# Performance work log

Hardware: AMD Instinct MI355X
Metric: run time of the kernel (lower is better)

The kernel has to match this reference:

```python
import jax, jax.numpy as jnp
import numpy as np

B, T, D, H, DH = 2, 2048, 1024, 16, 64
LN_EPS = 1e-5


def setup_inputs() -> dict:
    key = jax.random.key(0)
    ks = jax.random.split(key, 16)
    s = 0.02
    return {
        "query_sequences": jax.random.normal(ks[0], (B, T, D), jnp.float32),
        "key_sequences": jax.random.normal(ks[1], (B, T, D), jnp.float32),
        "value_sequences": jax.random.normal(ks[2], (B, T, D), jnp.float32),
        "key_value_sequence_lengths": jax.random.randint(ks[3], (B,), 1, T + 1),
        "Wq": jax.random.normal(ks[4], (D, H * DH), jnp.float32) * s,
        "bq": jnp.zeros((H * DH,), jnp.float32),
        "Wk": jax.random.normal(ks[5], (D, H * DH), jnp.float32) * s,
        "bk": jnp.zeros((H * DH,), jnp.float32),
        "Wv": jax.random.normal(ks[6], (D, H * DH), jnp.float32) * s,
        "bv": jnp.zeros((H * DH,), jnp.float32),
        "Wo": jax.random.normal(ks[7], (H * DH, D), jnp.float32) * s,
        "bo": jnp.zeros((D,), jnp.float32),
        "gamma": jnp.ones((D,), jnp.float32),
        "beta": jnp.zeros((D,), jnp.float32),
    }


def _layer_norm(x, gamma, beta):
    mu = jnp.mean(x, axis=-1, keepdims=True)
    var = jnp.var(x, axis=-1, keepdims=True)
    return (x - mu) * jax.lax.rsqrt(var + LN_EPS) * gamma + beta


def reference(query_sequences, key_sequences, value_sequences,
              key_value_sequence_lengths, Wq, bq, Wk, bk, Wv, bv, Wo, bo,
              gamma, beta):
    # pre-LN (self-attn: same LN applied to q, k, v inputs)
    q_in = _layer_norm(query_sequences, gamma, beta)
    k_in = _layer_norm(key_sequences, gamma, beta)
    v_in = _layer_norm(value_sequences, gamma, beta)

    # projections -> [B, H, T, DH]
    q = (q_in @ Wq + bq).reshape(B, T, H, DH).transpose(0, 2, 1, 3)
    k = (k_in @ Wk + bk).reshape(B, T, H, DH).transpose(0, 2, 1, 3)
    v = (v_in @ Wv + bv).reshape(B, T, H, DH).transpose(0, 2, 1, 3)

    scale = 1.0 / jnp.sqrt(jnp.float32(DH))
    scores = jnp.einsum('bhtd,bhTd->bhtT', q, k) * scale  # [B,H,Tq,Tk]

    # key padding mask: key position < sequence length
    pad_mask = jnp.arange(T)[None, None, None, :] < key_value_sequence_lengths[:, None, None, None]
    # causal mask (self_attn and in_decoder)
    causal = jnp.tril(jnp.ones((T, T), bool))[None, None]
    mask = pad_mask & causal
    scores = jnp.where(mask, scores, -jnp.inf)

    attn = jax.nn.softmax(scores, axis=-1)  # dropout=0 (eval)
    attn_viz = attn.reshape(B * H, T, T)

    out = jnp.einsum('bhtT,bhTd->bhtd', attn, v)
    out = out.transpose(0, 2, 1, 3).reshape(B, T, H * DH)
    out = out @ Wo + bo
    return out, attn_viz
```

## Files before the change

### kernel.cpp

```cpp
#include <hip/hip_runtime.h>
#include <hip/hip_bf16.h>

#define B_  2
#define T_  2048
#define D_  1024
#define H_  16
#define DH_ 64
#define M_  (B_*T_)

typedef __bf16 bf16;
typedef __bf16 bf16x8 __attribute__((ext_vector_type(8)));
typedef __bf16 bf16x4 __attribute__((ext_vector_type(4)));
typedef float  f32x4  __attribute__((ext_vector_type(4)));

#define SCL2 0.18033688011112042f

#define GLD16(g, l) __builtin_amdgcn_global_load_lds( \
    (const __attribute__((address_space(1))) void*)(g), \
    (__attribute__((address_space(3))) void*)(l), 16, 0, 0)

__global__ __launch_bounds__(256) void ln_kernel(
    const float* __restrict__ xq, const float* __restrict__ xk,
    const float* __restrict__ xv, const float* __restrict__ gamma,
    const float* __restrict__ beta,
    bf16* __restrict__ oq, bf16* __restrict__ ok, bf16* __restrict__ ov)
{
    const int row = blockIdx.x;
    const int sel = blockIdx.y;
    const float* x = (sel == 0 ? xq : sel == 1 ? xk : xv) + (size_t)row * D_;
    bf16*        o = (sel == 0 ? oq : sel == 1 ? ok : ov) + (size_t)row * D_;
    const int tid = threadIdx.x;

    float4 v = *(const float4*)&x[tid * 4];
    float s  = v.x + v.y + v.z + v.w;
    float s2 = v.x*v.x + v.y*v.y + v.z*v.z + v.w*v.w;
    for (int off = 32; off > 0; off >>= 1) {
        s  += __shfl_down(s,  off, 64);
        s2 += __shfl_down(s2, off, 64);
    }
    __shared__ float red[8];
    const int wave = tid >> 6, lane = tid & 63;
    if (lane == 0) { red[wave] = s; red[4 + wave] = s2; }
    __syncthreads();
    s  = red[0] + red[1] + red[2] + red[3];
    s2 = red[4] + red[5] + red[6] + red[7];
    const float mu   = s * (1.0f / D_);
    const float var  = s2 * (1.0f / D_) - mu * mu;
    const float rstd = rsqrtf(var + 1e-5f);

    float4 g  = *(const float4*)&gamma[tid * 4];
    float4 bb = *(const float4*)&beta[tid * 4];
    bf16x4 o4;
    o4[0] = (bf16)((v.x - mu) * rstd * g.x + bb.x);
    o4[1] = (bf16)((v.y - mu) * rstd * g.y + bb.y);
    o4[2] = (bf16)((v.z - mu) * rstd * g.z + bb.z);
    o4[3] = (bf16)((v.w - mu) * rstd * g.w + bb.w);
    *(bf16x4*)&o[tid * 4] = o4;
}

__global__ __launch_bounds__(256) void wconv_kernel(
    const float* __restrict__ Wq, const float* __restrict__ Wk,
    const float* __restrict__ Wv, const float* __restrict__ Wo,
    bf16* __restrict__ wqt, bf16* __restrict__ wkt,
    bf16* __restrict__ wvt, bf16* __restrict__ wot)
{
    const float* Ws[4] = {Wq, Wk, Wv, Wo};
    bf16*        Wt[4] = {wqt, wkt, wvt, wot};
    const float* W = Ws[blockIdx.z];
    bf16*        O = Wt[blockIdx.z];
    const int n0 = blockIdx.x * 32, k0 = blockIdx.y * 32;
    __shared__ float tile[32][33];
    const int tid = threadIdx.x;
    #pragma unroll
    for (int i = 0; i < 4; i++) {
        int e = tid + i * 256;
        int r = e >> 5, c = e & 31;
        tile[r][c] = W[(size_t)(k0 + r) * 1024 + n0 + c];
    }
    __syncthreads();
    #pragma unroll
    for (int i = 0; i < 4; i++) {
        int e = tid + i * 256;
        int nr = e >> 5, kc = e & 31;
        O[(size_t)(n0 + nr) * 1024 + k0 + kc] = (bf16)tile[kc][nr];
    }
}

__global__ __launch_bounds__(256) void vtrans_kernel(
    const bf16* __restrict__ Vh, bf16* __restrict__ VhT)
{
    const int bh = blockIdx.y, t0 = blockIdx.x * 64;
    const bf16* src = Vh  + (size_t)bh * T_ * DH_;
    bf16*       dst = VhT + (size_t)bh * T_ * DH_;
    __shared__ bf16 tile[64][72];
    const int tid = threadIdx.x;
    const int r = tid >> 3, c8 = (tid & 7) * 8;
    *(bf16x8*)&tile[r][c8]      = *(const bf16x8*)&src[(size_t)(t0 + r) * DH_ + c8];
    *(bf16x8*)&tile[32 + r][c8] = *(const bf16x8*)&src[(size_t)(t0 + 32 + r) * DH_ + c8];
    __syncthreads();
    bf16x8 o0, o1;
    #pragma unroll
    for (int j = 0; j < 8; j++) { o0[j] = tile[c8 + j][r]; o1[j] = tile[c8 + j][32 + r]; }
    *(bf16x8*)&dst[(size_t)r * T_ + t0 + c8]        = o0;
    *(bf16x8*)&dst[(size_t)(32 + r) * T_ + t0 + c8] = o1;
}

template <int MODE>
__global__ __launch_bounds__(256) void gemm_bt(
    const bf16* __restrict__ A, const bf16* __restrict__ Bt,
    const float* __restrict__ bias, void* __restrict__ Cout)
{
    __shared__ bf16 sA[128][32];
    __shared__ bf16 sB[128][32];
    const int tid  = threadIdx.x;
    const int wave = tid >> 6, lane = tid & 63;
    const int quad = lane >> 4, l16 = lane & 15;
    const int wr = (wave >> 1) * 64, wc = (wave & 1) * 64;
    const int m0 = blockIdx.y * 128, n0 = blockIdx.x * 128;

    f32x4 acc[4][4] = {};

    const int srow = wave * 32 + (lane >> 2);
    const int scol = (lane & 3) * 8;
    const bf16* gA0 = &A [(size_t)(m0 + srow)      * 1024 + scol];
    const bf16* gA1 = &A [(size_t)(m0 + srow + 16) * 1024 + scol];
    const bf16* gB0 = &Bt[(size_t)(n0 + srow)      * 1024 + scol];
    const bf16* gB1 = &Bt[(size_t)(n0 + srow + 16) * 1024 + scol];
    bf16* lA0 = &sA[wave * 32][0];
    bf16* lA1 = &sA[wave * 32 + 16][0];
    bf16* lB0 = &sB[wave * 32][0];
    bf16* lB1 = &sB[wave * 32 + 16][0];

    for (int k0 = 0; k0 < 1024; k0 += 32) {
        __syncthreads();
        GLD16(gA0 + k0, lA0);
        GLD16(gA1 + k0, lA1);
        GLD16(gB0 + k0, lB0);
        GLD16(gB1 + k0, lB1);
        __syncthreads();

        bf16x8 af[4], bfr[4];
        #pragma unroll
        for (int i = 0; i < 4; i++) af[i]  = *(bf16x8*)&sA[wr + i * 16 + l16][quad * 8];
        #pragma unroll
        for (int j = 0; j < 4; j++) bfr[j] = *(bf16x8*)&sB[wc + j * 16 + l16][quad * 8];
        #pragma unroll
        for (int i = 0; i < 4; i++)
            #pragma unroll
            for (int j = 0; j < 4; j++)
                acc[i][j] = __builtin_amdgcn_mfma_f32_16x16x32_bf16(af[i], bfr[j], acc[i][j], 0, 0, 0);
    }

    #pragma unroll
    for (int i = 0; i < 4; i++) {
        #pragma unroll
        for (int j = 0; j < 4; j++) {
            const int n = n0 + wc + j * 16 + l16;
            const float bia = bias[n];
            #pragma unroll
            for (int r = 0; r < 4; r++) {
                const int m = m0 + wr + i * 16 + quad * 4 + r;
                const float v = acc[i][j][r] + bia;
                if (MODE == 0) {
                    const int b = m >> 11, t = m & 2047, h = n >> 6, dh = n & 63;
                    ((bf16*)Cout)[(((size_t)b * H_ + h) * T_ + t) * DH_ + dh] = (bf16)v;
                } else {
                    ((float*)Cout)[(size_t)m * 1024 + n] = v;
                }
            }
        }
    }
}

__global__ __launch_bounds__(256) void attn_kernel(
    const bf16* __restrict__ Qh, const bf16* __restrict__ Kh,
    const bf16* __restrict__ VhT, const int* __restrict__ lens,
    float* __restrict__ attn_out, bf16* __restrict__ Obuf)
{
    const int bh = blockIdx.y;
    const int b = bh >> 4, h = bh & 15;
    const int bx = blockIdx.x;
    const int q0 = bx * 64;
    const int len = lens[b];
    const bf16* Qp = Qh  + (size_t)bh * T_ * DH_;
    const bf16* Kp = Kh  + (size_t)bh * T_ * DH_;
    const bf16* Vp = VhT + (size_t)bh * T_ * DH_;
    float* attnp = attn_out + (size_t)bh * T_ * T_;

    const int tid  = threadIdx.x;
    const int wave = tid >> 6, lane = tid & 63;
    const int quad = lane >> 4, l16 = lane & 15;

    __shared__ float Pf[4][16][68];

    const int qrow = q0 + wave * 16 + l16;
    const bf16x8 aq0 = *(const bf16x8*)&Qp[(size_t)qrow * DH_ + quad * 8];
    const bf16x8 aq1 = *(const bf16x8*)&Qp[(size_t)qrow * DH_ + 32 + quad * 8];

    const int jb_hi = min(bx, (len - 1) >> 6);

    float lsum[4] = {0.f, 0.f, 0.f, 0.f};

    for (int jb = 0; jb <= jb_hi; jb++) {
        f32x4 sc[4];
        #pragma unroll
        for (int c = 0; c < 4; c++) {
            const size_t krow = (size_t)(jb * 64 + c * 16 + l16) * DH_;
            bf16x8 b0 = *(const bf16x8*)&Kp[krow + quad * 8];
            bf16x8 b1 = *(const bf16x8*)&Kp[krow + 32 + quad * 8];
            f32x4 s = {};
            s = __builtin_amdgcn_mfma_f32_16x16x32_bf16(aq0, b0, s, 0, 0, 0);
            s = __builtin_amdgcn_mfma_f32_16x16x32_bf16(aq1, b1, s, 0, 0, 0);
            sc[c] = s;
        }
        if ((jb < bx) && ((jb + 1) * 64 <= len)) {
            #pragma unroll
            for (int c = 0; c < 4; c++)
                #pragma unroll
                for (int r = 0; r < 4; r++)
                    lsum[r] += __builtin_amdgcn_exp2f(sc[c][r] * SCL2);
        } else {
            #pragma unroll
            for (int c = 0; c < 4; c++) {
                const int k_g = jb * 64 + c * 16 + l16;
                #pragma unroll
                for (int r = 0; r < 4; r++) {
                    const int t_g = q0 + wave * 16 + quad * 4 + r;
                    const bool valid = (k_g <= t_g) & (k_g < len);
                    lsum[r] += valid ? __builtin_amdgcn_exp2f(sc[c][r] * SCL2) : 0.0f;
                }
            }
        }
    }
    float linv[4];
    #pragma unroll
    for (int r = 0; r < 4; r++) {
        float v = lsum[r];
        #pragma unroll
        for (int o = 1; o < 16; o <<= 1) v += __shfl_xor(v, o, 16);
        linv[r] = 1.0f / v;
    }

    f32x4 oacc[4] = {};
    for (int jb = 0; jb <= jb_hi; jb++) {
        f32x4 sc[4];
        #pragma unroll
        for (int c = 0; c < 4; c++) {
            const size_t krow = (size_t)(jb * 64 + c * 16 + l16) * DH_;
            bf16x8 b0 = *(const bf16x8*)&Kp[krow + quad * 8];
            bf16x8 b1 = *(const bf16x8*)&Kp[krow + 32 + quad * 8];
            f32x4 s = {};
            s = __builtin_amdgcn_mfma_f32_16x16x32_bf16(aq0, b0, s, 0, 0, 0);
            s = __builtin_amdgcn_mfma_f32_16x16x32_bf16(aq1, b1, s, 0, 0, 0);
            sc[c] = s;
        }
        const bool fullt = (jb < bx) && ((jb + 1) * 64 <= len);
        #pragma unroll
        for (int c = 0; c < 4; c++) {
            const int k_g = jb * 64 + c * 16 + l16;
            #pragma unroll
            for (int r = 0; r < 4; r++) {
                float p = __builtin_amdgcn_exp2f(sc[c][r] * SCL2) * linv[r];
                if (!fullt) {
                    const int t_g = q0 + wave * 16 + quad * 4 + r;
                    if (!((k_g <= t_g) & (k_g < len))) p = 0.0f;
                }
                Pf[wave][quad * 4 + r][c * 16 + l16] = p;
            }
        }
        asm volatile("s_waitcnt lgkmcnt(0)" ::: "memory");

        #pragma unroll
        for (int ks = 0; ks < 2; ks++) {
            f32x4 p0 = *(f32x4*)&Pf[wave][l16][ks * 32 + quad * 8];
            f32x4 p1 = *(f32x4*)&Pf[wave][l16][ks * 32 + quad * 8 + 4];
            bf16x8 ap;
            ap[0] = (bf16)p0[0]; ap[1] = (bf16)p0[1]; ap[2] = (bf16)p0[2]; ap[3] = (bf16)p0[3];
            ap[4] = (bf16)p1[0]; ap[5] = (bf16)p1[1]; ap[6] = (bf16)p1[2]; ap[7] = (bf16)p1[3];
            #pragma unroll
            for (int c = 0; c < 4; c++) {
                const bf16x8 vb = *(const bf16x8*)&Vp[(size_t)(c * 16 + l16) * T_ + jb * 64 + ks * 32 + quad * 8];
                oacc[c] = __builtin_amdgcn_mfma_f32_16x16x32_bf16(ap, vb, oacc[c], 0, 0, 0);
            }
        }

        #pragma unroll
        for (int s = 0; s < 4; s++) {
            const int row = s * 4 + (lane >> 4);
            const int c4  = (lane & 15) * 4;
            f32x4 v4 = *(f32x4*)&Pf[wave][row][c4];
            *(f32x4*)&attnp[(size_t)(q0 + wave * 16 + row) * T_ + jb * 64 + c4] = v4;
        }
    }

    const int zc0 = (jb_hi + 1) * 64;
    if (zc0 < T_) {
        const int span4 = (T_ - zc0) >> 2;
        for (int r = 0; r < 16; r++) {
            const size_t rowbase = (size_t)(q0 + wave * 16 + r) * T_ + zc0;
            for (int c4 = lane; c4 < span4; c4 += 64) {
                *(float4*)&attnp[rowbase + (size_t)c4 * 4] = make_float4(0.f, 0.f, 0.f, 0.f);
            }
        }
    }

    #pragma unroll
    for (int c = 0; c < 4; c++) {
        #pragma unroll
        for (int r = 0; r < 4; r++) {
            const int t_g = q0 + wave * 16 + quad * 4 + r;
            const int dh = c * 16 + l16;
            Obuf[(size_t)(b * T_ + t_g) * 1024 + h * DH_ + dh] = (bf16)oacc[c][r];
        }
    }
}

extern "C" void kernel_launch(void* const* d_in, const int* in_sizes, int n_in,
                              void* d_out, int out_size, void* d_ws, size_t ws_size,
                              hipStream_t stream)
{
    const float* xq    = (const float*)d_in[0];
    const float* xk    = (const float*)d_in[1];
    const float* xv    = (const float*)d_in[2];
    const int*   lens  = (const int*)d_in[3];
    const float* Wq    = (const float*)d_in[4];
    const float* bq    = (const float*)d_in[5];
    const float* Wk    = (const float*)d_in[6];
    const float* bk    = (const float*)d_in[7];
    const float* Wv    = (const float*)d_in[8];
    const float* bv    = (const float*)d_in[9];
    const float* Wo    = (const float*)d_in[10];
    const float* bo    = (const float*)d_in[11];
    const float* gamma = (const float*)d_in[12];
    const float* beta  = (const float*)d_in[13];

    float* out      = (float*)d_out;
    float* attn_out = out + (size_t)M_ * D_;

    char* ws = (char*)d_ws;
    bf16* lnq  = (bf16*)ws; ws += (size_t)M_ * D_ * 2;
    bf16* lnk  = (bf16*)ws; ws += (size_t)M_ * D_ * 2;
    bf16* lnv  = (bf16*)ws; ws += (size_t)M_ * D_ * 2;
    bf16* wqt  = (bf16*)ws; ws += (size_t)1024 * 1024 * 2;
    bf16* wkt  = (bf16*)ws; ws += (size_t)1024 * 1024 * 2;
    bf16* wvt  = (bf16*)ws; ws += (size_t)1024 * 1024 * 2;
    bf16* wot  = (bf16*)ws; ws += (size_t)1024 * 1024 * 2;
    bf16* Qh   = (bf16*)ws; ws += (size_t)M_ * D_ * 2;
    bf16* Kh   = (bf16*)ws; ws += (size_t)M_ * D_ * 2;
    bf16* Vh   = (bf16*)ws; ws += (size_t)M_ * D_ * 2;
    bf16* Obuf = (bf16*)ws; ws += (size_t)M_ * D_ * 2;
    bf16* VhT  = lnq;

    ln_kernel<<<dim3(M_, 3), 256, 0, stream>>>(xq, xk, xv, gamma, beta, lnq, lnk, lnv);
    wconv_kernel<<<dim3(32, 32, 4), 256, 0, stream>>>(Wq, Wk, Wv, Wo, wqt, wkt, wvt, wot);
    gemm_bt<0><<<dim3(8, 32), 256, 0, stream>>>(lnq, wqt, bq, (void*)Qh);
    gemm_bt<0><<<dim3(8, 32), 256, 0, stream>>>(lnk, wkt, bk, (void*)Kh);
    gemm_bt<0><<<dim3(8, 32), 256, 0, stream>>>(lnv, wvt, bv, (void*)Vh);
    vtrans_kernel<<<dim3(T_ / 64, B_ * H_), 256, 0, stream>>>(Vh, VhT);
    attn_kernel<<<dim3(T_ / 64, B_ * H_), 256, 0, stream>>>(Qh, Kh, VhT, lens, attn_out, Obuf);
    gemm_bt<1><<<dim3(8, 32), 256, 0, stream>>>(Obuf, wot, bo, (void*)out);
}
```

Measured before the change: 856.8 us.

## Batch QKV GEMMs, swizzle LDS tiles, stage K/V through shared memory in attention

Merges the three Q/K/V projection GEMMs into a single launch that picks the weight, bias and output slice from the row block, relying on contiguous lnq/lnk/lnv and wqt/wkt/wvt buffers. GEMM LDS tiles get an XOR swizzle to reduce bank conflicts, and the output GEMM uses 64-row tiles for more blocks. The attention kernel now loads K and V^T tiles cooperatively into swizzled shared memory instead of each wave reading them from global memory. This adds block-wide barriers per key tile and depends on the workspace buffers being laid out back to back.

```diff
diff --git a/kernel.cpp b/kernel.cpp
--- a/kernel.cpp
+++ b/kernel.cpp
@@ -105,65 +105,78 @@
     *(bf16x8*)&dst[(size_t)(32 + r) * T_ + t0 + c8] = o1;
 }
 
-template <int MODE>
+template <int TM, int MODE>
 __global__ __launch_bounds__(256) void gemm_bt(
-    const bf16* __restrict__ A, const bf16* __restrict__ Bt,
-    const float* __restrict__ bias, void* __restrict__ Cout)
-{
-    __shared__ bf16 sA[128][32];
-    __shared__ bf16 sB[128][32];
+    const bf16* __restrict__ A, const bf16* __restrict__ BtP,
+    const float* __restrict__ b0p, const float* __restrict__ b1p,
+    const float* __restrict__ b2p, void* __restrict__ Cout)
+{
+    __shared__ bf16 sA[TM * 32];
+    __shared__ bf16 sB[128 * 32];
     const int tid  = threadIdx.x;
     const int wave = tid >> 6, lane = tid & 63;
     const int quad = lane >> 4, l16 = lane & 15;
-    const int wr = (wave >> 1) * 64, wc = (wave & 1) * 64;
-    const int m0 = blockIdx.y * 128, n0 = blockIdx.x * 128;
-
-    f32x4 acc[4][4] = {};
-
-    const int srow = wave * 32 + (lane >> 2);
-    const int scol = (lane & 3) * 8;
-    const bf16* gA0 = &A [(size_t)(m0 + srow)      * 1024 + scol];
-    const bf16* gA1 = &A [(size_t)(m0 + srow + 16) * 1024 + scol];
-    const bf16* gB0 = &Bt[(size_t)(n0 + srow)      * 1024 + scol];
-    const bf16* gB1 = &Bt[(size_t)(n0 + srow + 16) * 1024 + scol];
-    bf16* lA0 = &sA[wave * 32][0];
-    bf16* lA1 = &sA[wave * 32 + 16][0];
-    bf16* lB0 = &sB[wave * 32][0];
-    bf16* lB1 = &sB[wave * 32 + 16][0];
+    const int m0 = blockIdx.y * TM, n0 = blockIdx.x * 128;
+    constexpr int MI = TM / 32;
+    const int wr = (wave >> 1) * (TM / 2), wc = (wave & 1) * 64;
+
+    const int sel = (MODE == 0) ? (m0 >> 12) : 0;
+    const bf16* Bt = BtP + (size_t)sel * 1024 * 1024;
+    const int mloc = (MODE == 0) ? (m0 & 4095) : m0;
+
+    f32x4 acc[MI][4] = {};
+    const int sr = lane >> 2;
+    const int su = lane & 3;
 
     for (int k0 = 0; k0 < 1024; k0 += 32) {
         __syncthreads();
-        GLD16(gA0 + k0, lA0);
-        GLD16(gA1 + k0, lA1);
-        GLD16(gB0 + k0, lB0);
-        GLD16(gB1 + k0, lB1);
-        __syncthreads();
-
-        bf16x8 af[4], bfr[4];
-        #pragma unroll
-        for (int i = 0; i < 4; i++) af[i]  = *(bf16x8*)&sA[wr + i * 16 + l16][quad * 8];
-        #pragma unroll
-        for (int j = 0; j < 4; j++) bfr[j] = *(bf16x8*)&sB[wc + j * 16 + l16][quad * 8];
-        #pragma unroll
-        for (int i = 0; i < 4; i++)
+        #pragma unroll
+        for (int i2 = 0; i2 < TM / 64; i2++) {
+            const int r = i2 * 64 + wave * 16 + sr;
+            GLD16(&A[(size_t)(m0 + r) * 1024 + k0 + (su ^ ((r >> 1) & 3)) * 8],
+                  &sA[(i2 * 256 + wave * 64) * 8]);
+        }
+        #pragma unroll
+        for (int i2 = 0; i2 < 2; i2++) {
+            const int r = i2 * 64 + wave * 16 + sr;
+            GLD16(&Bt[(size_t)(n0 + r) * 1024 + k0 + (su ^ ((r >> 1) & 3)) * 8],
+                  &sB[(i2 * 256 + wave * 64) * 8]);
+        }
+        __syncthreads();
+
+        bf16x8 af[MI], bfr[4];
+        #pragma unroll
+        for (int i = 0; i < MI; i++) {
+            const int row = wr + i * 16 + l16;
+            af[i] = *(bf16x8*)&sA[(row * 4 + (quad ^ ((row >> 1) & 3))) * 8];
+        }
+        #pragma unroll
+        for (int j = 0; j < 4; j++) {
+            const int row = wc + j * 16 + l16;
+            bfr[j] = *(bf16x8*)&sB[(row * 4 + (quad ^ ((row >> 1) & 3))) * 8];
+        }
+        #pragma unroll
+        for (int i = 0; i < MI; i++)
             #pragma unroll
             for (int j = 0; j < 4; j++)
                 acc[i][j] = __builtin_amdgcn_mfma_f32_16x16x32_bf16(af[i], bfr[j], acc[i][j], 0, 0, 0);
     }
 
-    #pragma unroll
-    for (int i = 0; i < 4; i++) {
+    const float* bias = (MODE == 0) ? (sel == 0 ? b0p : sel == 1 ? b1p : b2p) : b0p;
+    #pragma unroll
+    for (int i = 0; i < MI; i++) {
         #pragma unroll
         for (int j = 0; j < 4; j++) {
             const int n = n0 + wc + j * 16 + l16;
             const float bia = bias[n];
             #pragma unroll
             for (int r = 0; r < 4; r++) {
-                const int m = m0 + wr + i * 16 + quad * 4 + r;
+                const int m = mloc + wr + i * 16 + quad * 4 + r;
                 const float v = acc[i][j][r] + bia;
                 if (MODE == 0) {
                     const int b = m >> 11, t = m & 2047, h = n >> 6, dh = n & 63;
-                    ((bf16*)Cout)[(((size_t)b * H_ + h) * T_ + t) * DH_ + dh] = (bf16)v;
+                    ((bf16*)Cout)[(size_t)sel * M_ * D_ +
+                                  (((size_t)b * H_ + h) * T_ + t) * DH_ + dh] = (bf16)v;
                 } else {
                     ((float*)Cout)[(size_t)m * 1024 + n] = v;
                 }
@@ -191,6 +204,8 @@
     const int wave = tid >> 6, lane = tid & 63;
     const int quad = lane >> 4, l16 = lane & 15;
 
+    __shared__ bf16 sK[64 * 64];
+    __shared__ bf16 sV[64 * 64];
     __shared__ float Pf[4][16][68];
 
     const int qrow = q0 + wave * 16 + l16;
@@ -199,15 +214,27 @@
 
     const int jb_hi = min(bx, (len - 1) >> 6);
 
+    const int sr = lane >> 3;
+    const int su = lane & 7;
+
     float lsum[4] = {0.f, 0.f, 0.f, 0.f};
 
     for (int jb = 0; jb <= jb_hi; jb++) {
+        __syncthreads();
+        #pragma unroll
+        for (int i2 = 0; i2 < 2; i2++) {
+            const int r = i2 * 32 + wave * 8 + sr;
+            GLD16(&Kp[(size_t)(jb * 64 + r) * DH_ + (su ^ (r & 7)) * 8],
+                  &sK[(i2 * 256 + wave * 64) * 8]);
+        }
+        __syncthreads();
+
         f32x4 sc[4];
         #pragma unroll
         for (int c = 0; c < 4; c++) {
-            const size_t krow = (size_t)(jb * 64 + c * 16 + l16) * DH_;
-            bf16x8 b0 = *(const bf16x8*)&Kp[krow + quad * 8];
-            bf16x8 b1 = *(const bf16x8*)&Kp[krow + 32 + quad * 8];
+            const int row = c * 16 + l16;
+            bf16x8 b0 = *(bf16x8*)&sK[(row * 8 + (quad ^ (row & 7))) * 8];
+            bf16x8 b1 = *(bf16x8*)&sK[(row * 8 + ((quad + 4) ^ (row & 7))) * 8];
             f32x4 s = {};
             s = __builtin_amdgcn_mfma_f32_16x16x32_bf16(aq0, b0, s, 0, 0, 0);
             s = __builtin_amdgcn_mfma_f32_16x16x32_bf16(aq1, b1, s, 0, 0, 0);
@@ -243,12 +270,23 @@
 
     f32x4 oacc[4] = {};
     for (int jb = 0; jb <= jb_hi; jb++) {
+        __syncthreads();
+        #pragma unroll
+        for (int i2 = 0; i2 < 2; i2++) {
+            const int r = i2 * 32 + wave * 8 + sr;
+            GLD16(&Kp[(size_t)(jb * 64 + r) * DH_ + (su ^ (r & 7)) * 8],
+                  &sK[(i2 * 256 + wave * 64) * 8]);
+            GLD16(&Vp[(size_t)r * T_ + jb * 64 + (su ^ (r & 7)) * 8],
+                  &sV[(i2 * 256 + wave * 64) * 8]);
+        }
+        __syncthreads();
+
         f32x4 sc[4];
         #pragma unroll
         for (int c = 0; c < 4; c++) {
-            const size_t krow = (size_t)(jb * 64 + c * 16 + l16) * DH_;
-            bf16x8 b0 = *(const bf16x8*)&Kp[krow + quad * 8];
-            bf16x8 b1 = *(const bf16x8*)&Kp[krow + 32 + quad * 8];
+            const int row = c * 16 + l16;
+            bf16x8 b0 = *(bf16x8*)&sK[(row * 8 + (quad ^ (row & 7))) * 8];
+            bf16x8 b1 = *(bf16x8*)&sK[(row * 8 + ((quad + 4) ^ (row & 7))) * 8];
             f32x4 s = {};
             s = __builtin_amdgcn_mfma_f32_16x16x32_bf16(aq0, b0, s, 0, 0, 0);
             s = __builtin_amdgcn_mfma_f32_16x16x32_bf16(aq1, b1, s, 0, 0, 0);
@@ -279,7 +317,8 @@
             ap[4] = (bf16)p1[0]; ap[5] = (bf16)p1[1]; ap[6] = (bf16)p1[2]; ap[7] = (bf16)p1[3];
             #pragma unroll
             for (int c = 0; c < 4; c++) {
-                const bf16x8 vb = *(const bf16x8*)&Vp[(size_t)(c * 16 + l16) * T_ + jb * 64 + ks * 32 + quad * 8];
+                const int row = c * 16 + l16;
+                const bf16x8 vb = *(bf16x8*)&sV[(row * 8 + ((ks * 4 + quad) ^ (row & 7))) * 8];
                 oacc[c] = __builtin_amdgcn_mfma_f32_16x16x32_bf16(ap, vb, oacc[c], 0, 0, 0);
             }
         }
@@ -353,10 +392,8 @@
 
     ln_kernel<<<dim3(M_, 3), 256, 0, stream>>>(xq, xk, xv, gamma, beta, lnq, lnk, lnv);
     wconv_kernel<<<dim3(32, 32, 4), 256, 0, stream>>>(Wq, Wk, Wv, Wo, wqt, wkt, wvt, wot);
-    gemm_bt<0><<<dim3(8, 32), 256, 0, stream>>>(lnq, wqt, bq, (void*)Qh);
-    gemm_bt<0><<<dim3(8, 32), 256, 0, stream>>>(lnk, wkt, bk, (void*)Kh);
-    gemm_bt<0><<<dim3(8, 32), 256, 0, stream>>>(lnv, wvt, bv, (void*)Vh);
+    gemm_bt<128, 0><<<dim3(8, 96), 256, 0, stream>>>(lnq, wqt, bq, bk, bv, (void*)Qh);
     vtrans_kernel<<<dim3(T_ / 64, B_ * H_), 256, 0, stream>>>(Vh, VhT);
     attn_kernel<<<dim3(T_ / 64, B_ * H_), 256, 0, stream>>>(Qh, Kh, VhT, lens, attn_out, Obuf);
-    gemm_bt<1><<<dim3(8, 32), 256, 0, stream>>>(Obuf, wot, bo, (void*)out);
-}
+    gemm_bt<64, 1><<<dim3(8, 64), 256, 0, stream>>>(Obuf, wot, bo, bo, bo, (void*)out);
+}
```

Result: faster. 742.3 us (-13.4%).
